# Kernel optimization log

Hardware: AMD Instinct MI355X
Metric: run time of the kernel (lower is better)

## Reference

```python
import jax, jax.numpy as jnp
import numpy as np

B, C, N, K, COUT = 4, 64, 8192, 16, 64
EPS = 1e-5  # BatchNorm1d default eps


def setup_inputs() -> dict:
    key = jax.random.key(0)
    k1, k2, k3 = jax.random.split(key, 3)
    x = jax.random.normal(k1, (B, C, N), dtype=jnp.float32)
    coords = jax.random.normal(k2, (B, 3, N), dtype=jnp.float32)
    # Linear(2C -> COUT) params
    W = jax.random.normal(k3, (2 * C, COUT), dtype=jnp.float32) * (1.0 / np.sqrt(2 * C))
    b = jnp.zeros((COUT,), dtype=jnp.float32)
    # BatchNorm1d affine params (train-mode batch stats, as in torch default)
    gamma = jnp.ones((COUT,), dtype=jnp.float32)
    beta = jnp.zeros((COUT,), dtype=jnp.float32)
    return {"x": x, "coords": coords, "W": W, "b": b, "gamma": gamma, "beta": beta}


def reference(x, coords, W, b, gamma, beta):
    k = min(K, max(N - 1, 1))
    # --- kNN in coordinate space (squared distances give same ordering as cdist) ---
    ct = jnp.swapaxes(coords, 1, 2)                      # (B, N, 3)
    sq = jnp.sum(ct * ct, axis=-1)                       # (B, N)
    d2 = sq[:, :, None] + sq[:, None, :] - 2.0 * jnp.einsum('bnd,bmd->bnm', ct, ct)
    _, idx = jax.lax.top_k(-d2, k + 1)                   # smallest k+1 distances
    idx = idx[:, :, 1:]                                  # drop self -> (B, N, k)
    # --- gather neighbor features ---
    xt = jnp.swapaxes(x, 1, 2)                           # (B, N, C)
    nb = jax.vmap(lambda f, i: f[i])(xt, idx)            # (B, N, k, C)
    center = jnp.broadcast_to(xt[:, :, None, :], nb.shape)
    edge = jnp.concatenate([center, nb - center], axis=-1)  # (B, N, k, 2C)
    # --- edge MLP: Linear -> BatchNorm1d (batch stats) -> ReLU ---
    h = jnp.einsum('bnkc,cd->bnkd', edge, W) + b         # (B, N, k, COUT)
    mean = jnp.mean(h, axis=(0, 1, 2))
    var = jnp.var(h, axis=(0, 1, 2))
    h = (h - mean) * jax.lax.rsqrt(var + EPS) * gamma + beta
    h = jax.nn.relu(h)
    # --- max-pool over k neighbors ---
    out = jnp.max(h, axis=2)                             # (B, N, COUT)
    return jnp.swapaxes(out, 1, 2)                       # (B, COUT, N)
```

## Files before the change

### kernel.cpp

```cpp
#include <hip/hip_runtime.h>


#define Bn 4
#define Nn 8192
#define NSL 8
#define Gc 32
#define CS 32896
#define Hc 0.375f

typedef unsigned long long ull;

__device__ __forceinline__ int cellof(float v) {
  int i = (int)floorf((v + 6.0f) * (1.0f / Hc));
  return min(Gc - 1, max(0, i));
}

__global__ __launch_bounds__(256) void transpose_kernel(const float* __restrict__ x,
                                                        const float* __restrict__ coords,
                                                        float* __restrict__ xt,
                                                        float4* __restrict__ cpack) {
  __shared__ float tile[64][65];
  int bid = blockIdx.x;
  int b = bid >> 7;
  int n0 = (bid & 127) << 6;
  int tx = threadIdx.x & 63;
  int ty = threadIdx.x >> 6;
  for (int c = ty; c < 64; c += 4)
    tile[tx][c] = x[((size_t)b * 64 + c) * Nn + n0 + tx];
  if (ty == 0) {
    int n = n0 + tx;
    const float* cb = coords + (size_t)b * 3 * Nn;
    float cx = cb[n], cy = cb[Nn + n], cz = cb[2 * Nn + n];
    float cs = __fadd_rn(__fadd_rn(__fmul_rn(cx, cx), __fmul_rn(cy, cy)),
                         __fmul_rn(cz, cz));
    cpack[(size_t)b * Nn + n] = make_float4(cx, cy, cz, cs);
  }
  __syncthreads();
  for (int r = ty; r < 64; r += 4)
    xt[((size_t)b * Nn + n0 + r) * 64 + tx] = tile[r][tx];
}

__global__ __launch_bounds__(256) void hist_kernel(const float4* __restrict__ cpack,
                                                   unsigned* __restrict__ cells,
                                                   unsigned* __restrict__ cstart) {
  int n = blockIdx.x * 256 + threadIdx.x;
  float4 c = cpack[n];
  unsigned cell = ((unsigned)cellof(c.z) * Gc + cellof(c.y)) * Gc + cellof(c.x);
  cells[n] = cell;
  atomicAdd(&cstart[(unsigned)(n >> 13) * CS + cell], 1u);
}

__global__ __launch_bounds__(256) void scanA_kernel(unsigned* __restrict__ cstart,
                                                    unsigned* __restrict__ partials) {
  __shared__ unsigned sums[256];
  int bid = blockIdx.x, b = bid >> 4, ch = bid & 15, t = threadIdx.x;
  unsigned* base = cstart + (size_t)b * CS + ch * 2048 + t * 8;
  unsigned v[8], p = 0;
#pragma unroll
  for (int j = 0; j < 8; ++j) { unsigned c = base[j]; v[j] = p; p += c; }
  sums[t] = p;
  __syncthreads();
  for (int off = 1; off < 256; off <<= 1) {
    unsigned u = (t >= off) ? sums[t - off] : 0u;
    __syncthreads();
    sums[t] += u;
    __syncthreads();
  }
  unsigned excl = sums[t] - p;
#pragma unroll
  for (int j = 0; j < 8; ++j) base[j] = v[j] + excl;
  if (t == 255) partials[bid] = sums[255];
}

__global__ __launch_bounds__(256) void scanC_kernel(unsigned* __restrict__ cstart,
                                                    unsigned* __restrict__ cursor,
                                                    const unsigned* __restrict__ partials) {
  int bid = blockIdx.x, b = bid >> 4, ch = bid & 15, t = threadIdx.x;
  unsigned off = 0;
  for (int k = 0; k < ch; ++k) off += partials[b * 16 + k];
  size_t o = (size_t)b * CS + ch * 2048 + t * 8;
#pragma unroll
  for (int j = 0; j < 8; ++j) {
    unsigned val = cstart[o + j] + off;
    cstart[o + j] = val;
    cursor[o + j] = val;
  }
}

__global__ __launch_bounds__(256) void scatter_kernel(const float4* __restrict__ cpack,
                                                      const unsigned* __restrict__ cells,
                                                      unsigned* __restrict__ cursor,
                                                      float4* __restrict__ spos4,
                                                      unsigned* __restrict__ sidx) {
  int n = blockIdx.x * 256 + threadIdx.x;
  int b = n >> 13;
  unsigned slot = atomicAdd(&cursor[(size_t)b * CS + cells[n]], 1u);
  spos4[(size_t)b * Nn + slot] = cpack[n];
  sidx[(size_t)b * Nn + slot] = (unsigned)(n & 8191);
}

#define RMAX(kv) do {                                         \
    ull _kk = (kv);                                           \
    _Pragma("unroll")                                         \
    for (int _u = 0; _u < 16; ++_u)                           \
      ad[_u] = (ad[_u] == thr) ? _kk : ad[_u];                \
    ull _t0 = ad[0] > ad[1] ? ad[0] : ad[1];                  \
    ull _t1 = ad[2] > ad[3] ? ad[2] : ad[3];                  \
    ull _t2 = ad[4] > ad[5] ? ad[4] : ad[5];                  \
    ull _t3 = ad[6] > ad[7] ? ad[6] : ad[7];                  \
    ull _t4 = ad[8] > ad[9] ? ad[8] : ad[9];                  \
    ull _t5 = ad[10] > ad[11] ? ad[10] : ad[11];              \
    ull _t6 = ad[12] > ad[13] ? ad[12] : ad[13];              \
    ull _t7 = ad[14] > ad[15] ? ad[14] : ad[15];              \
    ull _u0 = _t0 > _t1 ? _t0 : _t1;                          \
    ull _u1 = _t2 > _t3 ? _t2 : _t3;                          \
    ull _u2 = _t4 > _t5 ? _t4 : _t5;                          \
    ull _u3 = _t6 > _t7 ? _t6 : _t7;                          \
    ull _v0 = _u0 > _u1 ? _u0 : _u1;                          \
    ull _v1 = _u2 > _u3 ? _u2 : _u3;                          \
    thr = _v0 > _v1 ? _v0 : _v1;                              \
  } while (0)

#define SINS(kv) do {                                         \
    ull _kk = (kv);                                           \
    if (_kk < nad[15]) {                                      \
      bool _ci = true;                                        \
      _Pragma("unroll")                                       \
      for (int _u = 15; _u >= 1; --_u) {                      \
        bool _cm = _kk < nad[_u - 1];                         \
        nad[_u] = _ci ? (_cm ? nad[_u - 1] : _kk) : nad[_u];  \
        _ci = _cm;                                            \
      }                                                       \
      nad[0] = _ci ? _kk : nad[0];                            \
    }                                                         \
  } while (0)

__global__ __launch_bounds__(512) void knn_kernel(const float4* __restrict__ spos4,
                                                  const unsigned* __restrict__ sidx,
                                                  int* __restrict__ knn) {
  __shared__ __align__(16) ull mk[(NSL - 1) * 16 * 64];
  float4* stage = (float4*)mk;
  unsigned* sixl = (unsigned*)(mk + 1024);
  __shared__ unsigned sthr[64];

  int bid = blockIdx.x;
  int b = bid >> 7;
  int grp = bid & 127;
  int tid = threadIdx.x;
  int lane = tid & 63;
  int s = tid >> 6;
  int qslot = grp * 64 + lane;

  const float4* sp = spos4 + (size_t)b * Nn;
  const unsigned* sx = sidx + (size_t)b * Nn;

  float4 qc = sp[qslot];
  unsigned qg = sx[qslot];
  float qs = qc.w;
  float qx2 = 2.f * qc.x, qy2 = 2.f * qc.y, qz2 = 2.f * qc.z;

  if (tid < 64) sthr[tid] = 0xFFFFFFFFu;

  ull ad[16];
#pragma unroll
  for (int i = 0; i < 16; ++i) ad[i] = 0xFFFFFFFF00000000ull | (unsigned)i;
  ull thr = 0xFFFFFFFF0000000Full;
  unsigned thr_hi = 0xFFFFFFFFu;

  int m0 = grp >> 3;
  int visited = 0;
  for (int step = 0; step < 32 && visited < 16; ++step) {
    int d = (step + 1) >> 1;
    int m = (step & 1) ? (m0 + d) : (m0 - d);
    if (m < 0 || m >= 16) continue;
    ++visited;

    __syncthreads();
    stage[tid] = sp[m * 512 + tid];
    sixl[tid] = sx[m * 512 + tid];
    __syncthreads();
#pragma unroll
    for (int half = 0; half < 2; ++half) {
      int loc = half * 256 + s * 32;
      int base = m * 512 + loc;
      unsigned sh = sthr[lane];
      thr_hi = sh < thr_hi ? sh : thr_hi;
      unsigned mask = 0;
#pragma unroll 8
      for (int j = 0; j < 32; ++j) {
        float4 c4 = stage[loc + j];
        float dot2 = __fadd_rn(__fadd_rn(__fmul_rn(qx2, c4.x), __fmul_rn(qy2, c4.y)),
                               __fmul_rn(qz2, c4.z));
        float d2 = __fsub_rn(__fadd_rn(qs, c4.w), dot2);
        mask |= (__float_as_uint(d2) <= thr_hi) ? (1u << j) : 0u;
      }
      unsigned sj = (unsigned)(qslot - base);
      if (sj < 32u) mask &= ~(1u << sj);
      while (__any(mask)) {
        if (mask) {
          int j = __ffs(mask) - 1;
          mask &= (mask - 1);
          float4 c4 = stage[loc + j];
          float dot2 = __fadd_rn(__fadd_rn(__fmul_rn(qx2, c4.x), __fmul_rn(qy2, c4.y)),
                                 __fmul_rn(qz2, c4.z));
          float d2 = __fsub_rn(__fadd_rn(qs, c4.w), dot2);
          ull key = ((ull)__float_as_uint(d2) << 32) | sixl[loc + j];
          if (key < thr) RMAX(key);
        }
      }
      unsigned lh = (unsigned)(thr >> 32);
      thr_hi = lh < thr_hi ? lh : thr_hi;
      atomicMin(&sthr[lane], lh);
    }
  }

  __syncthreads();
  if (s > 0) {
#pragma unroll
    for (int i = 0; i < 16; ++i) mk[(((s - 1) << 4) + i) * 64 + lane] = ad[i];
  }
  __syncthreads();
  if (s == 0) {
    ull nad[16];
#pragma unroll
    for (int i = 0; i < 16; ++i) nad[i] = ~0ull;
#pragma unroll
    for (int i = 0; i < 16; ++i) SINS(ad[i]);
    for (int t = 0; t < (NSL - 1) * 16; ++t) SINS(mk[t * 64 + lane]);
    int* op = knn + (size_t)(b * Nn + (int)qg) * 16;
#pragma unroll
    for (int i = 0; i < 16; ++i) op[i] = (int)(nad[i] & 0xFFFFFFFFull);
  }
}

__global__ __launch_bounds__(256) void edge_kernel(
    const float* __restrict__ xt, const int* __restrict__ knn,
    const float* __restrict__ W, const float* __restrict__ bias,
    float* __restrict__ mnb, float* __restrict__ mxb,
    float* __restrict__ ps1, float* __restrict__ ps2) {
  __shared__ float dlds[4][16][64];
  __shared__ float clds[4][64];
  __shared__ float r1[4][64], r2[4][64];

  int tid = threadIdx.x;
  int l = tid & 63;
  int w = tid >> 6;

  float w1[64], w2[64];
#pragma unroll
  for (int c = 0; c < 64; ++c) {
    w1[c] = W[c * 64 + l];
    w2[c] = W[(64 + c) * 64 + l];
  }
  float bl = bias[l];
  float s1 = 0.f, s2 = 0.f;

  int wid = blockIdx.x * 4 + w;
  int nw = gridDim.x * 4;
  for (int p = wid; p < Bn * Nn; p += nw) {
    int bb = p >> 13;
    const float* xb = xt + (size_t)bb * Nn * 64;
    float ctr = xt[(size_t)p * 64 + l];
    clds[w][l] = ctr;
    const int* ip = knn + (size_t)p * 16;
#pragma unroll
    for (int j = 0; j < 16; ++j) {
      int nj = ip[j];
      dlds[w][j][l] = xb[(size_t)nj * 64 + l] - ctr;
    }
    __syncthreads();

    float cc = bl;
#pragma unroll
    for (int c = 0; c < 64; ++c) cc = fmaf(clds[w][c], w1[c], cc);

    float mn = 3.0e38f, mx = -3.0e38f;
#pragma unroll
    for (int k = 0; k < 16; ++k) {
      float h = cc;
#pragma unroll
      for (int c = 0; c < 64; ++c) h = fmaf(dlds[w][k][c], w2[c], h);
      mn = fminf(mn, h);
      mx = fmaxf(mx, h);
      s1 += h;
      s2 = fmaf(h, h, s2);
    }
    mnb[(size_t)p * 64 + l] = mn;
    mxb[(size_t)p * 64 + l] = mx;
    __syncthreads();
  }

  r1[w][l] = s1; r2[w][l] = s2;
  __syncthreads();
  if (w == 0) {
    float a = r1[0][l] + r1[1][l] + r1[2][l] + r1[3][l];
    float c2 = r2[0][l] + r2[1][l] + r2[2][l] + r2[3][l];
    ps1[blockIdx.x * 64 + l] = a;
    ps2[blockIdx.x * 64 + l] = c2;
  }
}

__global__ __launch_bounds__(256) void stats_kernel(const float* __restrict__ ps1,
                                                    const float* __restrict__ ps2,
                                                    float* __restrict__ stats) {
  __shared__ float r1[4][64], r2[4][64];
  int c = threadIdx.x & 63, g = threadIdx.x >> 6;
  float a = 0.f, b2 = 0.f;
  for (int i = g; i < 512; i += 4) { a += ps1[i * 64 + c]; b2 += ps2[i * 64 + c]; }
  r1[g][c] = a; r2[g][c] = b2;
  __syncthreads();
  if (g == 0) {
    float s1 = r1[0][c] + r1[1][c] + r1[2][c] + r1[3][c];
    float s2 = r2[0][c] + r2[1][c] + r2[2][c] + r2[3][c];
    const float invM = 1.f / 524288.f;
    float mean = s1 * invM;
    float var = s2 * invM - mean * mean;
    stats[c] = mean;
    stats[64 + c] = var;
  }
}

__global__ __launch_bounds__(256) void final_kernel(
    const float* __restrict__ mnb, const float* __restrict__ mxb,
    const float* __restrict__ stats, const float* __restrict__ gamma,
    const float* __restrict__ beta, float* __restrict__ out) {
  __shared__ float tile[64][65];
  int bid = blockIdx.x;
  int b = bid >> 7;
  int n0 = (bid & 127) << 6;
  int tx = threadIdx.x & 63, ty = threadIdx.x >> 6;
  float mean = stats[tx], var = stats[64 + tx];
  float sc = gamma[tx] * rsqrtf(var + 1e-5f);
  float sh = fmaf(-mean, sc, beta[tx]);
  for (int r = ty; r < 64; r += 4) {
    size_t off = ((size_t)(b * Nn + n0 + r)) * 64 + tx;
    float lo = fmaf(mnb[off], sc, sh);
    float hi = fmaf(mxb[off], sc, sh);
    tile[tx][r] = fmaxf(fmaxf(hi, lo), 0.f);
  }
  __syncthreads();
  for (int r = ty; r < 64; r += 4)
    out[((size_t)b * 64 + r) * Nn + n0 + tx] = tile[r][tx];
}

extern "C" void kernel_launch(void* const* d_in, const int* in_sizes, int n_in,
                              void* d_out, int out_size, void* d_ws, size_t ws_size,
                              hipStream_t stream) {
  const float* x      = (const float*)d_in[0];
  const float* coords = (const float*)d_in[1];
  const float* W      = (const float*)d_in[2];
  const float* bias   = (const float*)d_in[3];
  const float* gamma  = (const float*)d_in[4];
  const float* beta   = (const float*)d_in[5];
  float* out = (float*)d_out;

  char* ws = (char*)d_ws;
  float*    xt       = (float*)ws;
  int*      knn      = (int*)(ws + 8388608);
  float*    mnb      = (float*)(ws + 10485760);
  float4*   cpack    = (float4*)(ws + 10485760);
  float*    mxb      = (float*)(ws + 18874368);
  float4*   spos4    = (float4*)(ws + 18874368);
  unsigned* cstart   = (unsigned*)(ws + 19398656);
  unsigned* cursor   = (unsigned*)(ws + 19924992);
  unsigned* cells    = (unsigned*)(ws + 20451328);
  unsigned* partials = (unsigned*)(ws + 20582400);
  unsigned* sidx     = (unsigned*)(ws + 20582656);
  float*    ps1      = (float*)(ws + 27262976);
  float*    ps2      = (float*)(ws + 27394048);
  float*    stats    = (float*)(ws + 27525120);

  transpose_kernel<<<dim3(512), dim3(256), 0, stream>>>(x, coords, xt, cpack);
  hipMemsetAsync(cstart, 0, (size_t)4 * CS * 4, stream);
  hist_kernel<<<dim3(128), dim3(256), 0, stream>>>(cpack, cells, cstart);
  scanA_kernel<<<dim3(64), dim3(256), 0, stream>>>(cstart, partials);
  scanC_kernel<<<dim3(64), dim3(256), 0, stream>>>(cstart, cursor, partials);
  scatter_kernel<<<dim3(128), dim3(256), 0, stream>>>(cpack, cells, cursor, spos4, sidx);
  knn_kernel<<<dim3(512), dim3(512), 0, stream>>>(spos4, sidx, knn);
  edge_kernel<<<dim3(512), dim3(256), 0, stream>>>(xt, knn, W, bias, mnb, mxb, ps1, ps2);
  stats_kernel<<<dim3(1), dim3(256), 0, stream>>>(ps1, ps2, stats);
  final_kernel<<<dim3(512), dim3(256), 0, stream>>>(mnb, mxb, stats, gamma, beta, out);
}
```

Measured before the change: 579.0 us.

## Prune kNN candidate chunks using per-chunk bounding boxes

A new kernel computes an axis-aligned bounding box for each 512-point chunk of the spatially sorted coordinates. Before staging a chunk, the kNN kernel computes each query's minimum squared distance to that chunk's box. It skips the chunk when every lane in the wavefront already has a current k-th distance threshold below that bound. This avoids loading and distance-testing chunks that cannot hold any neighbour, at the cost of one small extra kernel launch and a per-chunk bounds check.

```diff
diff --git a/kernel.cpp b/kernel.cpp
--- a/kernel.cpp
+++ b/kernel.cpp
@@ -97,6 +97,27 @@
   unsigned slot = atomicAdd(&cursor[(size_t)b * CS + cells[n]], 1u);
   spos4[(size_t)b * Nn + slot] = cpack[n];
   sidx[(size_t)b * Nn + slot] = (unsigned)(n & 8191);
+}
+
+__global__ __launch_bounds__(256) void bbox_kernel(const float4* __restrict__ spos4,
+                                                   float4* __restrict__ bbox) {
+  __shared__ float4 smn[256], smx[256];
+  int blk = blockIdx.x;
+  int t = threadIdx.x;
+  const float4* sp = spos4 + (size_t)(blk >> 4) * Nn + (blk & 15) * 512;
+  float4 a = sp[t], c = sp[t + 256];
+  smn[t] = make_float4(fminf(a.x, c.x), fminf(a.y, c.y), fminf(a.z, c.z), 0.f);
+  smx[t] = make_float4(fmaxf(a.x, c.x), fmaxf(a.y, c.y), fmaxf(a.z, c.z), 0.f);
+  __syncthreads();
+  for (int off = 128; off > 0; off >>= 1) {
+    if (t < off) {
+      float4 n2 = smn[t + off], x2 = smx[t + off], n1 = smn[t], x1 = smx[t];
+      smn[t] = make_float4(fminf(n1.x, n2.x), fminf(n1.y, n2.y), fminf(n1.z, n2.z), 0.f);
+      smx[t] = make_float4(fmaxf(x1.x, x2.x), fmaxf(x1.y, x2.y), fmaxf(x1.z, x2.z), 0.f);
+    }
+    __syncthreads();
+  }
+  if (t == 0) { bbox[blk * 2] = smn[0]; bbox[blk * 2 + 1] = smx[0]; }
 }
 
 #define RMAX(kv) do {                                         \
@@ -137,6 +158,7 @@
 
 __global__ __launch_bounds__(512) void knn_kernel(const float4* __restrict__ spos4,
                                                   const unsigned* __restrict__ sidx,
+                                                  const float4* __restrict__ bbox,
                                                   int* __restrict__ knn) {
   __shared__ __align__(16) ull mk[(NSL - 1) * 16 * 64];
   float4* stage = (float4*)mk;
@@ -176,6 +198,17 @@
     ++visited;
 
     __syncthreads();
+
+    float4 bmn = bbox[(b * 16 + m) * 2];
+    float4 bmx = bbox[(b * 16 + m) * 2 + 1];
+    float ddx = fmaxf(fmaxf(bmn.x - qc.x, qc.x - bmx.x), 0.f);
+    float ddy = fmaxf(fmaxf(bmn.y - qc.y, qc.y - bmx.y), 0.f);
+    float ddz = fmaxf(fmaxf(bmn.z - qc.z, qc.z - bmx.z), 0.f);
+    float dmin2 = ddx * ddx + ddy * ddy + ddz * ddz;
+    unsigned shu = sthr[lane];
+    int skipl = (dmin2 > __uint_as_float(shu) + 1e-3f) ? 1 : 0;
+    if (__all(skipl)) continue;
+
     stage[tid] = sp[m * 512 + tid];
     sixl[tid] = sx[m * 512 + tid];
     __syncthreads();
@@ -366,6 +399,7 @@
   unsigned* cells    = (unsigned*)(ws + 20451328);
   unsigned* partials = (unsigned*)(ws + 20582400);
   unsigned* sidx     = (unsigned*)(ws + 20582656);
+  float4*   bbox     = (float4*)(ws + 20713728);
   float*    ps1      = (float*)(ws + 27262976);
   float*    ps2      = (float*)(ws + 27394048);
   float*    stats    = (float*)(ws + 27525120);
@@ -376,7 +410,8 @@
   scanA_kernel<<<dim3(64), dim3(256), 0, stream>>>(cstart, partials);
   scanC_kernel<<<dim3(64), dim3(256), 0, stream>>>(cstart, cursor, partials);
   scatter_kernel<<<dim3(128), dim3(256), 0, stream>>>(cpack, cells, cursor, spos4, sidx);
-  knn_kernel<<<dim3(512), dim3(512), 0, stream>>>(spos4, sidx, knn);
+  bbox_kernel<<<dim3(64), dim3(256), 0, stream>>>(spos4, bbox);
+  knn_kernel<<<dim3(512), dim3(512), 0, stream>>>(spos4, sidx, bbox, knn);
   edge_kernel<<<dim3(512), dim3(256), 0, stream>>>(xt, knn, W, bias, mnb, mxb, ps1, ps2);
   stats_kernel<<<dim3(1), dim3(256), 0, stream>>>(ps1, ps2, stats);
   final_kernel<<<dim3(512), dim3(256), 0, stream>>>(mnb, mxb, stats, gamma, beta, out);
```

Result: no change. 588.4 us (+1.6%).
